# Kernel optimization log

Hardware: AMD Instinct MI355X
Metric: run time of the kernel (lower is better)

Reference implementation:

```python
import jax, jax.numpy as jnp
import numpy as np

T, H, I = 4096, 4096, 11008  # tokens, hidden, intermediate


def setup_inputs() -> dict:
    key = jax.random.key(0)
    k = jax.random.split(key, 6)
    # int8-range quantized activations and weights (stored as int32 for jax matmul)
    x_q = jax.random.randint(k[0], (T, H), -127, 128).astype(jnp.int32)
    w_gate_up = jax.random.randint(k[1], (2 * I, H), -127, 128).astype(jnp.int32)
    w_down = jax.random.randint(k[2], (H, I), -127, 128).astype(jnp.int32)
    # per-token dynamic input scale, per-output-channel weight scales
    x_scale = jax.random.uniform(k[3], (T,), jnp.float32, 1e-4, 2e-2)
    s_w_gate_up = jax.random.uniform(k[4], (2 * I,), jnp.float32, 1e-4, 2e-2)
    s_w_down = jax.random.uniform(k[5], (H,), jnp.float32, 1e-4, 2e-2)
    return {"x_q": x_q, "x_scale": x_scale, "w_gate_up": w_gate_up,
            "s_w_gate_up": s_w_gate_up, "w_down": w_down, "s_w_down": s_w_down}


def reference(x_q, x_scale, w_gate_up, s_w_gate_up, w_down, s_w_down):
    # --- gate_up_proj: W8A8 int8 GEMM + dequant (per-token x per-channel scales) ---
    gu_i32 = jnp.matmul(x_q, w_gate_up.T)                                   # [T, 2I] int32 accum
    gu = gu_i32.astype(jnp.float32) * x_scale[:, None] * s_w_gate_up[None, :]
    gate, up = gu[:, :I], gu[:, I:]
    # --- SiluAndMulQuant: fused SiLU(gate)*up + per-token dynamic requant to int8 ---
    y = jax.nn.silu(gate) * up                                              # [T, I] fp
    s2 = jnp.maximum(jnp.max(jnp.abs(y), axis=-1), 1e-8) / 127.0            # [T] new dynamic scale
    y_q = jnp.clip(jnp.round(y / s2[:, None]), -128.0, 127.0).astype(jnp.int32)
    # --- down_proj: W8A8 int8 GEMM + dequant ---
    out_i32 = jnp.matmul(y_q, w_down.T)                                     # [T, H] int32 accum
    out = out_i32.astype(jnp.float32) * s2[:, None] * s_w_down[None, :]
    return out
```

## Files before the change

kernel.cpp:

```cpp
#include <hip/hip_runtime.h>
#include <cstdint>
#include <cstddef>

#define T_DIM 4096
#define H_DIM 4096
#define I_DIM 11008

typedef int v4i __attribute__((ext_vector_type(4)));

__device__ __forceinline__ void async_copy16(const void* g, void* l) {
  __builtin_amdgcn_global_load_lds(
      (const __attribute__((address_space(1))) void*)g,
      (__attribute__((address_space(3))) void*)l, 16, 0, 0);
}

__global__ void pack_i8(const int4* __restrict__ src, char4* __restrict__ dst, int n4) {
  int stride = gridDim.x * blockDim.x;
  for (int i = blockIdx.x * blockDim.x + threadIdx.x; i < n4; i += stride) {
    int4 v = src[i];
    char4 c;
    c.x = (char)v.x; c.y = (char)v.y; c.z = (char)v.z; c.w = (char)v.w;
    dst[i] = c;
  }
}

__global__ void zero_u32(unsigned* __restrict__ p, int n) {
  int i = blockIdx.x * blockDim.x + threadIdx.x;
  if (i < n) p[i] = 0u;
}

__global__ __launch_bounds__(256, 2)
void gemm1_silu(const int8_t* __restrict__ x8,
                const int8_t* __restrict__ wgu8,
                const float* __restrict__ x_scale,
                const float* __restrict__ s_wgu,
                float* __restrict__ y,
                unsigned* __restrict__ rowmax) {
  __shared__ __align__(16) char lds0[24576];
  __shared__ __align__(16) char lds1[24576];
  __shared__ __align__(16) char lds2[24576];

  const int tid = threadIdx.x;
  const int wave = tid >> 6, lane = tid & 63;
  const int wm = wave >> 1, wn = wave & 1;

  const unsigned bid = blockIdx.y * gridDim.x + blockIdx.x;
  const unsigned xcd = bid & 7;
  const unsigned l   = bid >> 3;
  const unsigned s   = l >> 5;
  const unsigned r   = l - (s << 5);
  const int m0 = (int)(xcd * 4 + (r & 3)) * 128;
  const int n0 = (int)(s * 8 + (r >> 2)) * 128;

  v4i accg[4][4], accu[4][4];
  const v4i vzero = {0, 0, 0, 0};
#pragma unroll
  for (int i = 0; i < 4; i++)
#pragma unroll
    for (int j = 0; j < 4; j++) { accg[i][j] = vzero; accu[i][j] = vzero; }

  const int8_t* Ab  = x8 + (size_t)m0 * H_DIM;
  const int8_t* Bgb = wgu8 + (size_t)n0 * H_DIM;
  const int8_t* Bub = wgu8 + ((size_t)I_DIM + (size_t)n0) * H_DIM;

  const int sr0 = wave * 16 + (lane >> 2);
  const int sr1 = (4 + wave) * 16 + (lane >> 2);
  const int sc0 = (lane & 3) ^ ((sr0 >> 1) & 3);
  const int sc1 = (lane & 3) ^ ((sr1 >> 1) & 3);
  const size_t vo0 = (size_t)sr0 * H_DIM + (size_t)sc0 * 16;
  const size_t vo1 = (size_t)sr1 * H_DIM + (size_t)sc1 * 16;
  const int ldsSeg0 = wave * 1024;
  const int ldsSeg1 = (4 + wave) * 1024;

  const int cfrag = ((lane >> 4) ^ (((lane & 15) >> 1) & 3)) * 16;
  const int aoff = (wm * 64 + (lane & 15)) * 64 + cfrag;
  const int boff = (wn * 64 + (lane & 15)) * 64 + cfrag;

#define G1_STAGE(L, T)                                                      \
  {                                                                         \
    const int8_t* A_ = Ab + ((size_t)(T) << 6);                             \
    const int8_t* G_ = Bgb + ((size_t)(T) << 6);                            \
    const int8_t* U_ = Bub + ((size_t)(T) << 6);                            \
    async_copy16(A_ + vo0, (L) + ldsSeg0);                                  \
    async_copy16(A_ + vo1, (L) + ldsSeg1);                                  \
    async_copy16(G_ + vo0, (L) + 8192 + ldsSeg0);                           \
    async_copy16(G_ + vo1, (L) + 8192 + ldsSeg1);                           \
    async_copy16(U_ + vo0, (L) + 16384 + ldsSeg0);                          \
    async_copy16(U_ + vo1, (L) + 16384 + ldsSeg1);                          \
  }

#define G1_PHASE(Lc, Ls, T2, DOSTAGE, VM)                                   \
  {                                                                         \
    v4i a[4], bg[4], bu[4];                                                 \
    _Pragma("unroll")                                                       \
    for (int i = 0; i < 4; i++) a[i]  = *(const v4i*)((Lc) + aoff + i * 1024);          \
    _Pragma("unroll")                                                       \
    for (int j = 0; j < 4; j++) bg[j] = *(const v4i*)((Lc) + 8192 + boff + j * 1024);   \
    _Pragma("unroll")                                                       \
    for (int j = 0; j < 4; j++) bu[j] = *(const v4i*)((Lc) + 16384 + boff + j * 1024);  \
    if (DOSTAGE) G1_STAGE(Ls, T2);                                          \
    __builtin_amdgcn_s_setprio(1);                                          \
    _Pragma("unroll")                                                       \
    for (int i = 0; i < 4; i++)                                             \
      _Pragma("unroll")                                                     \
      for (int j = 0; j < 4; j++) {                                         \
        accg[i][j] = __builtin_amdgcn_mfma_i32_16x16x64_i8(a[i], bg[j], accg[i][j], 0, 0, 0); \
        accu[i][j] = __builtin_amdgcn_mfma_i32_16x16x64_i8(a[i], bu[j], accu[i][j], 0, 0, 0); \
      }                                                                     \
    __builtin_amdgcn_s_setprio(0);                                          \
    asm volatile("s_waitcnt " VM ::: "memory");                             \
    __builtin_amdgcn_s_barrier();                                           \
  }

  G1_STAGE(lds0, 0);
  G1_STAGE(lds1, 1);
  asm volatile("s_waitcnt vmcnt(6)" ::: "memory");
  __builtin_amdgcn_s_barrier();

  for (int t = 0; t < 60; t += 3) {
    G1_PHASE(lds0, lds2, t + 2, 1, "vmcnt(6)")
    G1_PHASE(lds1, lds0, t + 3, 1, "vmcnt(6)")
    G1_PHASE(lds2, lds1, t + 4, 1, "vmcnt(6)")
  }
  G1_PHASE(lds0, lds2, 62, 1, "vmcnt(6)")
  G1_PHASE(lds1, lds0, 63, 1, "vmcnt(6)")
  G1_PHASE(lds2, lds0,  0, 0, "vmcnt(0)")
  G1_PHASE(lds0, lds0,  0, 0, "vmcnt(0)")
#undef G1_PHASE
#undef G1_STAGE

  const int lr = lane >> 4;
  const int lc = lane & 15;
#pragma unroll
  for (int i = 0; i < 4; i++) {
#pragma unroll
    for (int t = 0; t < 4; t++) {
      const int gr = m0 + wm * 64 + i * 16 + lr * 4 + t;
      const float sx = x_scale[gr];
      float vmax = 0.f;
#pragma unroll
      for (int j = 0; j < 4; j++) {
        const int gc = n0 + wn * 64 + j * 16 + lc;
        float g = (float)accg[i][j][t] * sx * s_wgu[gc];
        float u = (float)accu[i][j][t] * sx * s_wgu[I_DIM + gc];
        float yv = (g / (1.f + expf(-g))) * u;
        y[(size_t)gr * I_DIM + gc] = yv;
        vmax = fmaxf(vmax, fabsf(yv));
      }
#pragma unroll
      for (int off = 1; off < 16; off <<= 1)
        vmax = fmaxf(vmax, __shfl_xor(vmax, off, 64));
      if (lc == 0) atomicMax(&rowmax[gr], __float_as_uint(vmax));
    }
  }
}

__global__ void quantize_y(const float* __restrict__ y,
                           const unsigned* __restrict__ rowmax,
                           int8_t* __restrict__ yq) {
  size_t gid = (size_t)blockIdx.x * blockDim.x + threadIdx.x;
  size_t base = gid * 4;
  if (base >= (size_t)T_DIM * I_DIM) return;
  int row = (int)(base / I_DIM);
  float inv = 127.f / fmaxf(__uint_as_float(rowmax[row]), 1e-8f);
  float4 v = *(const float4*)(y + base);
  char4 q;
  q.x = (char)(int)fminf(127.f, fmaxf(-128.f, rintf(v.x * inv)));
  q.y = (char)(int)fminf(127.f, fmaxf(-128.f, rintf(v.y * inv)));
  q.z = (char)(int)fminf(127.f, fmaxf(-128.f, rintf(v.z * inv)));
  q.w = (char)(int)fminf(127.f, fmaxf(-128.f, rintf(v.w * inv)));
  *(char4*)(yq + base) = q;
}

__global__ __launch_bounds__(256, 3)
void gemm2_scaled(const int8_t* __restrict__ yq8,
                  const int8_t* __restrict__ wd8,
                  const unsigned* __restrict__ rowmax,
                  const float* __restrict__ s_wd,
                  float* __restrict__ out) {
  __shared__ __align__(16) char lds0[16384];
  __shared__ __align__(16) char lds1[16384];
  __shared__ __align__(16) char lds2[16384];

  const int tid = threadIdx.x;
  const int wave = tid >> 6, lane = tid & 63;
  const int wm = wave >> 1, wn = wave & 1;

  const unsigned bid = blockIdx.y * gridDim.x + blockIdx.x;
  const unsigned xcd = bid & 7;
  const unsigned l   = bid >> 3;
  const unsigned s   = l >> 5;
  const unsigned r   = l & 31;
  const int m0 = (int)(xcd * 4 + (r & 3)) * 128;
  const int n0 = (int)(s * 8 + (r >> 2)) * 128;

  v4i acc[4][4];
  const v4i vzero = {0, 0, 0, 0};
#pragma unroll
  for (int i = 0; i < 4; i++)
#pragma unroll
    for (int j = 0; j < 4; j++) acc[i][j] = vzero;

  const int8_t* Ab = yq8 + (size_t)m0 * I_DIM;
  const int8_t* Bb = wd8 + (size_t)n0 * I_DIM;

  const int sr0 = wave * 16 + (lane >> 2);
  const int sr1 = (4 + wave) * 16 + (lane >> 2);
  const int sc0 = (lane & 3) ^ ((sr0 >> 1) & 3);
  const int sc1 = (lane & 3) ^ ((sr1 >> 1) & 3);
  const size_t vo0 = (size_t)sr0 * I_DIM + (size_t)sc0 * 16;
  const size_t vo1 = (size_t)sr1 * I_DIM + (size_t)sc1 * 16;
  const int ldsSeg0 = wave * 1024;
  const int ldsSeg1 = (4 + wave) * 1024;

  const int cfrag = ((lane >> 4) ^ (((lane & 15) >> 1) & 3)) * 16;
  const int aoff = (wm * 64 + (lane & 15)) * 64 + cfrag;
  const int boff = (wn * 64 + (lane & 15)) * 64 + cfrag;

#define G2_STAGE(L, T)                                                      \
  {                                                                         \
    const int8_t* A_ = Ab + ((size_t)(T) << 6);                             \
    const int8_t* B_ = Bb + ((size_t)(T) << 6);                             \
    async_copy16(A_ + vo0, (L) + ldsSeg0);                                  \
    async_copy16(A_ + vo1, (L) + ldsSeg1);                                  \
    async_copy16(B_ + vo0, (L) + 8192 + ldsSeg0);                           \
    async_copy16(B_ + vo1, (L) + 8192 + ldsSeg1);                           \
  }

#define G2_PHASE(Lc, Ls, T2, DOSTAGE, VM)                                   \
  {                                                                         \
    v4i a[4], b[4];                                                         \
    _Pragma("unroll")                                                       \
    for (int i = 0; i < 4; i++) a[i] = *(const v4i*)((Lc) + aoff + i * 1024);        \
    _Pragma("unroll")                                                       \
    for (int j = 0; j < 4; j++) b[j] = *(const v4i*)((Lc) + 8192 + boff + j * 1024); \
    if (DOSTAGE) G2_STAGE(Ls, T2);                                          \
    __builtin_amdgcn_s_setprio(1);                                          \
    _Pragma("unroll")                                                       \
    for (int i = 0; i < 4; i++)                                             \
      _Pragma("unroll")                                                     \
      for (int j = 0; j < 4; j++)                                           \
        acc[i][j] = __builtin_amdgcn_mfma_i32_16x16x64_i8(a[i], b[j], acc[i][j], 0, 0, 0); \
    __builtin_amdgcn_s_setprio(0);                                          \
    asm volatile("s_waitcnt " VM ::: "memory");                             \
    __builtin_amdgcn_s_barrier();                                           \
  }

  G2_STAGE(lds0, 0);
  G2_STAGE(lds1, 1);
  asm volatile("s_waitcnt vmcnt(4)" ::: "memory");
  __builtin_amdgcn_s_barrier();

  for (int t = 0; t < 168; t += 3) {
    G2_PHASE(lds0, lds2, t + 2, 1, "vmcnt(4)")
    G2_PHASE(lds1, lds0, t + 3, 1, "vmcnt(4)")
    G2_PHASE(lds2, lds1, t + 4, 1, "vmcnt(4)")
  }
  G2_PHASE(lds0, lds2, 170, 1, "vmcnt(4)")
  G2_PHASE(lds1, lds0, 171, 1, "vmcnt(4)")
  G2_PHASE(lds2, lds0,   0, 0, "vmcnt(0)")
  G2_PHASE(lds0, lds0,   0, 0, "vmcnt(0)")
#undef G2_PHASE
#undef G2_STAGE

  const int lr = lane >> 4;
  const int lc = lane & 15;
#pragma unroll
  for (int i = 0; i < 4; i++) {
#pragma unroll
    for (int t = 0; t < 4; t++) {
      const int gr = m0 + wm * 64 + i * 16 + lr * 4 + t;
      const float s2 = fmaxf(__uint_as_float(rowmax[gr]), 1e-8f) / 127.f;
#pragma unroll
      for (int j = 0; j < 4; j++) {
        const int gc = n0 + wn * 64 + j * 16 + lc;
        out[(size_t)gr * H_DIM + gc] = (float)acc[i][j][t] * s2 * s_wd[gc];
      }
    }
  }
}

extern "C" void kernel_launch(void* const* d_in, const int* in_sizes, int n_in,
                              void* d_out, int out_size, void* d_ws, size_t ws_size,
                              hipStream_t stream) {
  const int*   x_q     = (const int*)d_in[0];
  const float* x_scale = (const float*)d_in[1];
  const int*   w_gu    = (const int*)d_in[2];
  const float* s_wgu   = (const float*)d_in[3];
  const int*   w_d     = (const int*)d_in[4];
  const float* s_wd    = (const float*)d_in[5];
  float* out = (float*)d_out;

  char* ws = (char*)d_ws;
  const size_t SZ_X8   = (size_t)T_DIM * H_DIM;
  const size_t SZ_WGU8 = (size_t)2 * I_DIM * H_DIM;
  const size_t SZ_WD8  = (size_t)H_DIM * I_DIM;
  const size_t SZ_Y    = (size_t)T_DIM * I_DIM * 4;
  const size_t SZ_YQ   = (size_t)T_DIM * I_DIM;

  int8_t*   x8     = (int8_t*)ws;
  int8_t*   wgu8   = (int8_t*)(ws + SZ_X8);
  int8_t*   wd8    = (int8_t*)(ws + SZ_X8 + SZ_WGU8);
  float*    y      = (float*)(ws + SZ_X8 + SZ_WGU8 + SZ_WD8);
  int8_t*   yq8    = (int8_t*)(ws + SZ_X8 + SZ_WGU8 + SZ_WD8 + SZ_Y);
  unsigned* rowmax = (unsigned*)(ws + SZ_X8 + SZ_WGU8 + SZ_WD8 + SZ_Y + SZ_YQ);

  pack_i8<<<dim3(8192), dim3(256), 0, stream>>>((const int4*)x_q,  (char4*)x8,   (int)(SZ_X8 / 4));
  pack_i8<<<dim3(8192), dim3(256), 0, stream>>>((const int4*)w_gu, (char4*)wgu8, (int)(SZ_WGU8 / 4));
  pack_i8<<<dim3(8192), dim3(256), 0, stream>>>((const int4*)w_d,  (char4*)wd8,  (int)(SZ_WD8 / 4));
  zero_u32<<<dim3(16), dim3(256), 0, stream>>>(rowmax, T_DIM);

  gemm1_silu<<<dim3(I_DIM / 128, T_DIM / 128), dim3(256), 0, stream>>>(
      x8, wgu8, x_scale, s_wgu, y, rowmax);

  quantize_y<<<dim3((unsigned)((size_t)T_DIM * I_DIM / 4 / 256)), dim3(256), 0, stream>>>(
      y, rowmax, yq8);

  gemm2_scaled<<<dim3(H_DIM / 128, T_DIM / 128), dim3(256), 0, stream>>>(
      yq8, wd8, rowmax, s_wd, out);
}
```

Baseline: 1.321 ms.

## Widen down-proj GEMM tile to 128x256 with doubled per-wave accumulators

The down-projection int8 GEMM tile grows from 128x128 to 128x256. Each wave now accumulates 4x8 MFMA fragments, and each stage loads twice as many B rows into larger triple-buffered LDS. This raises arithmetic intensity and halves redundant A-tile reads, which should cut global/LDS traffic per MFMA. In exchange it uses more registers and LDS, lowering occupancy (launch bounds drop to 2) and halving the grid to 512 blocks. The block-to-tile mapping is also simplified.

```diff
diff --git a/kernel.cpp b/kernel.cpp
--- a/kernel.cpp
+++ b/kernel.cpp
@@ -172,15 +172,15 @@
   *(char4*)(yq + base) = q;
 }
 
-__global__ __launch_bounds__(256, 3)
+__global__ __launch_bounds__(256, 2)
 void gemm2_scaled(const int8_t* __restrict__ yq8,
                   const int8_t* __restrict__ wd8,
                   const unsigned* __restrict__ rowmax,
                   const float* __restrict__ s_wd,
                   float* __restrict__ out) {
-  __shared__ __align__(16) char lds0[16384];
-  __shared__ __align__(16) char lds1[16384];
-  __shared__ __align__(16) char lds2[16384];
+  __shared__ __align__(16) char lds0[24576];
+  __shared__ __align__(16) char lds1[24576];
+  __shared__ __align__(16) char lds2[24576];
 
   const int tid = threadIdx.x;
   const int wave = tid >> 6, lane = tid & 63;
@@ -189,57 +189,63 @@
   const unsigned bid = blockIdx.y * gridDim.x + blockIdx.x;
   const unsigned xcd = bid & 7;
   const unsigned l   = bid >> 3;
-  const unsigned s   = l >> 5;
-  const unsigned r   = l & 31;
-  const int m0 = (int)(xcd * 4 + (r & 3)) * 128;
-  const int n0 = (int)(s * 8 + (r >> 2)) * 128;
-
-  v4i acc[4][4];
+  const int m0 = (int)(xcd * 4 + (l & 3)) * 128;
+  const int n0 = (int)(l >> 2) * 256;
+
+  v4i acc[4][8];
   const v4i vzero = {0, 0, 0, 0};
 #pragma unroll
   for (int i = 0; i < 4; i++)
 #pragma unroll
-    for (int j = 0; j < 4; j++) acc[i][j] = vzero;
+    for (int j = 0; j < 8; j++) acc[i][j] = vzero;
 
   const int8_t* Ab = yq8 + (size_t)m0 * I_DIM;
   const int8_t* Bb = wd8 + (size_t)n0 * I_DIM;
 
-  const int sr0 = wave * 16 + (lane >> 2);
-  const int sr1 = (4 + wave) * 16 + (lane >> 2);
-  const int sc0 = (lane & 3) ^ ((sr0 >> 1) & 3);
-  const int sc1 = (lane & 3) ^ ((sr1 >> 1) & 3);
-  const size_t vo0 = (size_t)sr0 * I_DIM + (size_t)sc0 * 16;
-  const size_t vo1 = (size_t)sr1 * I_DIM + (size_t)sc1 * 16;
-  const int ldsSeg0 = wave * 1024;
-  const int ldsSeg1 = (4 + wave) * 1024;
+  const int lrow = lane >> 2;
+  const int lchk = lane & 3;
+  int srA[2], srB[4];
+  srA[0] = wave * 16 + lrow;        srA[1] = (4 + wave) * 16 + lrow;
+#pragma unroll
+  for (int q = 0; q < 4; q++) srB[q] = (q * 4 + wave) * 16 + lrow;
+  size_t voA[2], voB[4];
+#pragma unroll
+  for (int q = 0; q < 2; q++)
+    voA[q] = (size_t)srA[q] * I_DIM + (size_t)(lchk ^ ((srA[q] >> 1) & 3)) * 16;
+#pragma unroll
+  for (int q = 0; q < 4; q++)
+    voB[q] = (size_t)srB[q] * I_DIM + (size_t)(lchk ^ ((srB[q] >> 1) & 3)) * 16;
+  const int segA0 = wave * 1024, segA1 = (4 + wave) * 1024;
 
   const int cfrag = ((lane >> 4) ^ (((lane & 15) >> 1) & 3)) * 16;
   const int aoff = (wm * 64 + (lane & 15)) * 64 + cfrag;
-  const int boff = (wn * 64 + (lane & 15)) * 64 + cfrag;
+  const int boff = (wn * 128 + (lane & 15)) * 64 + cfrag;
 
 #define G2_STAGE(L, T)                                                      \
   {                                                                         \
     const int8_t* A_ = Ab + ((size_t)(T) << 6);                             \
     const int8_t* B_ = Bb + ((size_t)(T) << 6);                             \
-    async_copy16(A_ + vo0, (L) + ldsSeg0);                                  \
-    async_copy16(A_ + vo1, (L) + ldsSeg1);                                  \
-    async_copy16(B_ + vo0, (L) + 8192 + ldsSeg0);                           \
-    async_copy16(B_ + vo1, (L) + 8192 + ldsSeg1);                           \
+    async_copy16(A_ + voA[0], (L) + segA0);                                 \
+    async_copy16(A_ + voA[1], (L) + segA1);                                 \
+    async_copy16(B_ + voB[0], (L) + 8192 + segA0);                          \
+    async_copy16(B_ + voB[1], (L) + 8192 + segA1);                          \
+    async_copy16(B_ + voB[2], (L) + 8192 + segA0 + 8192);                   \
+    async_copy16(B_ + voB[3], (L) + 8192 + segA1 + 8192);                   \
   }
 
 #define G2_PHASE(Lc, Ls, T2, DOSTAGE, VM)                                   \
   {                                                                         \
-    v4i a[4], b[4];                                                         \
+    v4i a[4], b[8];                                                         \
     _Pragma("unroll")                                                       \
     for (int i = 0; i < 4; i++) a[i] = *(const v4i*)((Lc) + aoff + i * 1024);        \
     _Pragma("unroll")                                                       \
-    for (int j = 0; j < 4; j++) b[j] = *(const v4i*)((Lc) + 8192 + boff + j * 1024); \
+    for (int j = 0; j < 8; j++) b[j] = *(const v4i*)((Lc) + 8192 + boff + j * 1024); \
     if (DOSTAGE) G2_STAGE(Ls, T2);                                          \
     __builtin_amdgcn_s_setprio(1);                                          \
     _Pragma("unroll")                                                       \
     for (int i = 0; i < 4; i++)                                             \
       _Pragma("unroll")                                                     \
-      for (int j = 0; j < 4; j++)                                           \
+      for (int j = 0; j < 8; j++)                                           \
         acc[i][j] = __builtin_amdgcn_mfma_i32_16x16x64_i8(a[i], b[j], acc[i][j], 0, 0, 0); \
     __builtin_amdgcn_s_setprio(0);                                          \
     asm volatile("s_waitcnt " VM ::: "memory");                             \
@@ -248,16 +254,16 @@
 
   G2_STAGE(lds0, 0);
   G2_STAGE(lds1, 1);
-  asm volatile("s_waitcnt vmcnt(4)" ::: "memory");
+  asm volatile("s_waitcnt vmcnt(6)" ::: "memory");
   __builtin_amdgcn_s_barrier();
 
   for (int t = 0; t < 168; t += 3) {
-    G2_PHASE(lds0, lds2, t + 2, 1, "vmcnt(4)")
-    G2_PHASE(lds1, lds0, t + 3, 1, "vmcnt(4)")
-    G2_PHASE(lds2, lds1, t + 4, 1, "vmcnt(4)")
-  }
-  G2_PHASE(lds0, lds2, 170, 1, "vmcnt(4)")
-  G2_PHASE(lds1, lds0, 171, 1, "vmcnt(4)")
+    G2_PHASE(lds0, lds2, t + 2, 1, "vmcnt(6)")
+    G2_PHASE(lds1, lds0, t + 3, 1, "vmcnt(6)")
+    G2_PHASE(lds2, lds1, t + 4, 1, "vmcnt(6)")
+  }
+  G2_PHASE(lds0, lds2, 170, 1, "vmcnt(6)")
+  G2_PHASE(lds1, lds0, 171, 1, "vmcnt(6)")
   G2_PHASE(lds2, lds0,   0, 0, "vmcnt(0)")
   G2_PHASE(lds0, lds0,   0, 0, "vmcnt(0)")
 #undef G2_PHASE
@@ -272,8 +278,8 @@
       const int gr = m0 + wm * 64 + i * 16 + lr * 4 + t;
       const float s2 = fmaxf(__uint_as_float(rowmax[gr]), 1e-8f) / 127.f;
 #pragma unroll
-      for (int j = 0; j < 4; j++) {
-        const int gc = n0 + wn * 64 + j * 16 + lc;
+      for (int j = 0; j < 8; j++) {
+        const int gc = n0 + wn * 128 + j * 16 + lc;
         out[(size_t)gr * H_DIM + gc] = (float)acc[i][j][t] * s2 * s_wd[gc];
       }
     }
@@ -316,6 +322,6 @@
   quantize_y<<<dim3((unsigned)((size_t)T_DIM * I_DIM / 4 / 256)), dim3(256), 0, stream>>>(
       y, rowmax, yq8);
 
-  gemm2_scaled<<<dim3(H_DIM / 128, T_DIM / 128), dim3(256), 0, stream>>>(
+  gemm2_scaled<<<dim3(H_DIM / 256, T_DIM / 128), dim3(256), 0, stream>>>(
       yq8, wd8, rowmax, s_wd, out);
 }
```

Result: faster. 1.288 ms (-2.5%).
